# Performance work log

Measured on AMD Instinct MI355X. Metric: run time of the kernel, lower is better.

The kernel has to match this reference:

```python
import jax, jax.numpy as jnp
import numpy as np

N_NODES = 100000
N_EDGES = 1600000
IN_DIM = 256
HEADS = 4
OUT_DIM = 32
ALPHA = 0.2  # leaky relu slope


def setup_inputs() -> dict:
    key = jax.random.key(0)
    k1, k2, k3, k4, k5, k6 = jax.random.split(key, 6)
    feature = jax.random.normal(k1, (N_NODES, IN_DIM), dtype=jnp.float32)
    src = jax.random.randint(k2, (N_EDGES,), 0, N_NODES, dtype=jnp.int32)
    dst = jax.random.randint(k3, (N_EDGES,), 0, N_NODES, dtype=jnp.int32)
    W_fc = jax.random.normal(k4, (IN_DIM, HEADS * OUT_DIM), dtype=jnp.float32) * 0.05
    attn_l = jax.random.normal(k5, (1, HEADS, OUT_DIM), dtype=jnp.float32) * 0.1
    attn_r = jax.random.normal(k6, (1, HEADS, OUT_DIM), dtype=jnp.float32) * 0.1
    return {"feature": feature, "src": src, "dst": dst, "W_fc": W_fc,
            "attn_l": attn_l, "attn_r": attn_r}


def reference(feature, src, dst, W_fc, attn_l, attn_r):
    # node projection: [N, H, D]
    ft = (feature @ W_fc).reshape(feature.shape[0], HEADS, OUT_DIM)
    # per-node attention scores: [N, H]
    a1 = jnp.sum(ft * attn_l, axis=-1)
    a2 = jnp.sum(ft * attn_r, axis=-1)
    # edge attention logits: gather src/dst + leaky relu -> [E, H]
    e = a1[src] + a2[dst]
    e = jnp.where(e > 0, e, ALPHA * e)
    # segment softmax over destination groups
    n = feature.shape[0]
    e_max = jax.ops.segment_max(e, dst, num_segments=n)  # [N, H]
    e_exp = jnp.exp(e - e_max[dst])
    e_sum = jax.ops.segment_sum(e_exp, dst, num_segments=n)  # [N, H]
    alpha = e_exp / e_sum[dst]  # [E, H]
    # weighted scatter-sum aggregation: [N, H, D]
    msgs = ft[src] * alpha[:, :, None]
    out = jax.ops.segment_sum(msgs, dst, num_segments=n)
    return out
```

## Files before the change

kernel.cpp:

```cpp
#include <hip/hip_runtime.h>
#include <hip/hip_fp16.h>

#define N_NODES 100000
#define N_EDGES 1600000
#define IN_DIM 256
#define HEADS 4
#define OUT_DIM 32
#define NHD 128
#define LEAKY 0.2f

#define SCAN_BLOCK 1024
#define N_SCAN_BLOCKS ((N_NODES + SCAN_BLOCK - 1) / SCAN_BLOCK)

typedef _Float16 f16x8 __attribute__((ext_vector_type(8)));
typedef _Float16 f16x4 __attribute__((ext_vector_type(4)));
typedef float    f32x4 __attribute__((ext_vector_type(4)));

__global__ void init_kernel(int* __restrict__ deg) {
    int i = blockIdx.x * blockDim.x + threadIdx.x;
    if (i < N_NODES) deg[i] = 0;
}

__global__ void wprep_kernel(const float* __restrict__ W,
                             _Float16* __restrict__ Wt_hi,
                             _Float16* __restrict__ Wt_lo) {
    int i = blockIdx.x * blockDim.x + threadIdx.x;
    if (i < NHD * IN_DIM) {
        int c = i >> 8;
        int k = i & 255;
        float w = W[(size_t)k * NHD + c];
        _Float16 hi = (_Float16)w;
        _Float16 lo = (_Float16)(w - (float)hi);
        Wt_hi[i] = hi;
        Wt_lo[i] = lo;
    }
}

__launch_bounds__(256, 4)
__global__ void gemm_kernel(const float* __restrict__ feature,
                            const _Float16* __restrict__ Wt_hi,
                            const _Float16* __restrict__ Wt_lo,
                            const float* __restrict__ attn_l,
                            const float* __restrict__ attn_r,
                            __half* __restrict__ ft,
                            float* __restrict__ a1,
                            float* __restrict__ a2) {
    __shared__ _Float16 sA [128][40];
    __shared__ _Float16 sWh[128][40];
    __shared__ _Float16 sWl[128][40];

    const int t    = threadIdx.x;
    const int w    = t >> 6;
    const int lane = t & 63;
    const int l15  = lane & 15;
    const int kg   = lane >> 4;
    const int nb   = blockIdx.x * 128;

    f32x4 acc[8][2];
#pragma unroll
    for (int nt = 0; nt < 8; ++nt) {
        acc[nt][0] = (f32x4){0.f, 0.f, 0.f, 0.f};
        acc[nt][1] = (f32x4){0.f, 0.f, 0.f, 0.f};
    }

    for (int kt = 0; kt < 8; ++kt) {
        __syncthreads();
#pragma unroll
        for (int p = 0; p < 4; ++p) {
            int idx  = t + p * 256;
            int node = idx >> 3;
            int c4   = idx & 7;
            float4 v = make_float4(0.f, 0.f, 0.f, 0.f);
            if (nb + node < N_NODES)
                v = *(const float4*)&feature[(size_t)(nb + node) * IN_DIM + kt * 32 + c4 * 4];
            f16x4 h;
            h[0] = (_Float16)v.x; h[1] = (_Float16)v.y;
            h[2] = (_Float16)v.z; h[3] = (_Float16)v.w;
            *(f16x4*)&sA[node][c4 * 4] = h;
        }
#pragma unroll
        for (int p = 0; p < 2; ++p) {
            int c   = t + p * 256;
            int col = c >> 2;
            int kc  = c & 3;
            *(f16x8*)&sWh[col][kc * 8] =
                *(const f16x8*)&Wt_hi[(size_t)col * IN_DIM + kt * 32 + kc * 8];
            *(f16x8*)&sWl[col][kc * 8] =
                *(const f16x8*)&Wt_lo[(size_t)col * IN_DIM + kt * 32 + kc * 8];
        }
        __syncthreads();

        f16x8 wh0 = *(const f16x8*)&sWh[w * 32 + l15][kg * 8];
        f16x8 wh1 = *(const f16x8*)&sWh[w * 32 + 16 + l15][kg * 8];
        f16x8 wl0 = *(const f16x8*)&sWl[w * 32 + l15][kg * 8];
        f16x8 wl1 = *(const f16x8*)&sWl[w * 32 + 16 + l15][kg * 8];

#pragma unroll
        for (int nt = 0; nt < 8; ++nt) {
            f16x8 af = *(const f16x8*)&sA[nt * 16 + l15][kg * 8];
            acc[nt][0] = __builtin_amdgcn_mfma_f32_16x16x32_f16(wh0, af, acc[nt][0], 0, 0, 0);
            acc[nt][0] = __builtin_amdgcn_mfma_f32_16x16x32_f16(wl0, af, acc[nt][0], 0, 0, 0);
            acc[nt][1] = __builtin_amdgcn_mfma_f32_16x16x32_f16(wh1, af, acc[nt][1], 0, 0, 0);
            acc[nt][1] = __builtin_amdgcn_mfma_f32_16x16x32_f16(wl1, af, acc[nt][1], 0, 0, 0);
        }
    }

    float al8[8], ar8[8];
#pragma unroll
    for (int ct = 0; ct < 2; ++ct)
#pragma unroll
        for (int r = 0; r < 4; ++r) {
            int cb = ct * 16 + kg * 4 + r;
            al8[ct * 4 + r] = attn_l[w * 32 + cb];
            ar8[ct * 4 + r] = attn_r[w * 32 + cb];
        }

#pragma unroll
    for (int nt = 0; nt < 8; ++nt) {
        int node = nb + nt * 16 + l15;
        bool valid = node < N_NODES;
        if (valid) {
            f16x4 s0, s1;
#pragma unroll
            for (int r = 0; r < 4; ++r) {
                s0[r] = (_Float16)acc[nt][0][r];
                s1[r] = (_Float16)acc[nt][1][r];
            }
            *(f16x4*)&ft[(size_t)node * NHD + w * 32 + kg * 4]      = s0;
            *(f16x4*)&ft[(size_t)node * NHD + w * 32 + 16 + kg * 4] = s1;
        }
        float pl = 0.f, pr = 0.f;
#pragma unroll
        for (int ct = 0; ct < 2; ++ct)
#pragma unroll
            for (int r = 0; r < 4; ++r) {
                pl = fmaf(acc[nt][ct][r], al8[ct * 4 + r], pl);
                pr = fmaf(acc[nt][ct][r], ar8[ct * 4 + r], pr);
            }
        pl += __shfl_xor(pl, 16); pl += __shfl_xor(pl, 32);
        pr += __shfl_xor(pr, 16); pr += __shfl_xor(pr, 32);
        if (kg == 0 && valid) {
            a1[node * HEADS + w] = pl;
            a2[node * HEADS + w] = pr;
        }
    }
}

__global__ void hist_kernel(const int* __restrict__ dst, int* __restrict__ deg,
                            int* __restrict__ edge_pos) {
    int i = blockIdx.x * blockDim.x + threadIdx.x;
    if (i < N_EDGES) edge_pos[i] = atomicAdd(&deg[dst[i]], 1);
}

__global__ void scan1_kernel(const int* __restrict__ deg,
                             int* __restrict__ partial,
                             int* __restrict__ blocksum) {
    __shared__ int wsum[16];
    const int tid  = threadIdx.x;
    const int lane = tid & 63;
    const int wid  = tid >> 6;
    const int i    = blockIdx.x * SCAN_BLOCK + tid;
    int v = (i < N_NODES) ? deg[i] : 0;
    int x = v;
#pragma unroll
    for (int o = 1; o < 64; o <<= 1) {
        int y = __shfl_up(x, o);
        if (lane >= o) x += y;
    }
    if (lane == 63) wsum[wid] = x;
    __syncthreads();
    if (wid == 0 && lane < 16) {
        int w = wsum[lane];
#pragma unroll
        for (int o = 1; o < 16; o <<= 1) {
            int y = __shfl_up(w, o);
            if (lane >= o) w += y;
        }
        wsum[lane] = w;
    }
    __syncthreads();
    int woff = (wid > 0) ? wsum[wid - 1] : 0;
    if (i < N_NODES) partial[i] = woff + x - v;
    if (tid == SCAN_BLOCK - 1) blocksum[blockIdx.x] = wsum[15];
}

__global__ void scan2_kernel(const int* __restrict__ blocksum,
                             int* __restrict__ blockoff,
                             int* __restrict__ offsets) {
    __shared__ int wtot[2];
    const int tid  = threadIdx.x;
    const int lane = tid & 63;
    const int wid  = tid >> 6;
    int v = (tid < N_SCAN_BLOCKS) ? blocksum[tid] : 0;
    int x = v;
#pragma unroll
    for (int o = 1; o < 64; o <<= 1) {
        int y = __shfl_up(x, o);
        if (lane >= o) x += y;
    }
    if (lane == 63) wtot[wid] = x;
    __syncthreads();
    int add = (wid == 1) ? wtot[0] : 0;
    if (tid < N_SCAN_BLOCKS) blockoff[tid] = add + x - v;
    if (tid == N_SCAN_BLOCKS - 1) offsets[N_NODES] = add + x;
}

__global__ void scan3_kernel(const int* __restrict__ partial,
                             const int* __restrict__ blockoff,
                             int* __restrict__ offsets) {
    int i = blockIdx.x * SCAN_BLOCK + threadIdx.x;
    if (i < N_NODES) offsets[i] = partial[i] + blockoff[blockIdx.x];
}

__global__ void fill_kernel(const int* __restrict__ src, const int* __restrict__ dst,
                            const int* __restrict__ offsets,
                            const int* __restrict__ edge_pos,
                            int* __restrict__ src_sorted) {
    int i = blockIdx.x * blockDim.x + threadIdx.x;
    if (i < N_EDGES) {
        int idx = offsets[dst[i]] + edge_pos[i];
        src_sorted[idx] = src[i];
    }
}

__launch_bounds__(256)
__global__ void agg_kernel(const __half* __restrict__ ft,
                           const float* __restrict__ a1,
                           const float* __restrict__ a2,
                           const int* __restrict__ offsets,
                           const int* __restrict__ src_sorted,
                           float* __restrict__ out) {
    const int wave = threadIdx.x >> 6;
    const int lane = threadIdx.x & 63;
    const int node = blockIdx.x * 4 + wave;
    if (node >= N_NODES) return;
    const int h = lane >> 4;

    const float a2v = a2[node * HEADS + h];
    const int e0 = offsets[node];
    const int e1 = offsets[node + 1];

    float accx = 0.f, accy = 0.f, wsum = 0.f;
    int e = e0;

    for (; e + 3 < e1; e += 4) {
        int s0 = src_sorted[e];
        int s1 = src_sorted[e + 1];
        int s2 = src_sorted[e + 2];
        int s3 = src_sorted[e + 3];
        float b0 = a1[s0 * HEADS + h];
        float b1 = a1[s1 * HEADS + h];
        float b2 = a1[s2 * HEADS + h];
        float b3 = a1[s3 * HEADS + h];
        __half2 h0 = *(const __half2*)&ft[(size_t)s0 * NHD + lane * 2];
        __half2 h1 = *(const __half2*)&ft[(size_t)s1 * NHD + lane * 2];
        __half2 h2 = *(const __half2*)&ft[(size_t)s2 * NHD + lane * 2];
        __half2 h3 = *(const __half2*)&ft[(size_t)s3 * NHD + lane * 2];
        float2 v0 = __half22float2(h0);
        float2 v1 = __half22float2(h1);
        float2 v2 = __half22float2(h2);
        float2 v3 = __half22float2(h3);
        float ev0 = b0 + a2v; ev0 = ev0 > 0.f ? ev0 : LEAKY * ev0;
        float ev1 = b1 + a2v; ev1 = ev1 > 0.f ? ev1 : LEAKY * ev1;
        float ev2 = b2 + a2v; ev2 = ev2 > 0.f ? ev2 : LEAKY * ev2;
        float ev3 = b3 + a2v; ev3 = ev3 > 0.f ? ev3 : LEAKY * ev3;
        float w0 = __expf(ev0), w1 = __expf(ev1), w2 = __expf(ev2), w3 = __expf(ev3);
        accx = fmaf(w0, v0.x, accx); accy = fmaf(w0, v0.y, accy);
        accx = fmaf(w1, v1.x, accx); accy = fmaf(w1, v1.y, accy);
        accx = fmaf(w2, v2.x, accx); accy = fmaf(w2, v2.y, accy);
        accx = fmaf(w3, v3.x, accx); accy = fmaf(w3, v3.y, accy);
        wsum += w0 + w1 + w2 + w3;
    }
    for (; e < e1; ++e) {
        int s    = src_sorted[e];
        float ev = a1[s * HEADS + h] + a2v;
        ev       = ev > 0.f ? ev : LEAKY * ev;
        float w  = __expf(ev);
        float2 v = __half22float2(*(const __half2*)&ft[(size_t)s * NHD + lane * 2]);
        accx = fmaf(w, v.x, accx);
        accy = fmaf(w, v.y, accy);
        wsum += w;
    }
    float inv = (e1 > e0) ? 1.f / wsum : 0.f;
    float2 o = make_float2(accx * inv, accy * inv);
    *(float2*)&out[(size_t)node * NHD + lane * 2] = o;
}

extern "C" void kernel_launch(void* const* d_in, const int* in_sizes, int n_in,
                              void* d_out, int out_size, void* d_ws, size_t ws_size,
                              hipStream_t stream) {
    const float* feature = (const float*)d_in[0];
    const int*   src     = (const int*)d_in[1];
    const int*   dst     = (const int*)d_in[2];
    const float* W       = (const float*)d_in[3];
    const float* attn_l  = (const float*)d_in[4];
    const float* attn_r  = (const float*)d_in[5];
    float*       out     = (float*)d_out;

    char* ws = (char*)d_ws;
    size_t off = 0;
    auto alloc = [&](size_t bytes) -> void* {
        void* p = ws + off;
        off = (off + bytes + 255) & ~(size_t)255;
        return p;
    };
    __half*    ft        = (__half*)alloc((size_t)N_NODES * NHD * 2);
    float*     a1        = (float*)alloc((size_t)N_NODES * HEADS * 4);
    float*     a2        = (float*)alloc((size_t)N_NODES * HEADS * 4);
    int*       deg       = (int*)alloc((size_t)N_NODES * 4);
    int*       offsets   = (int*)alloc((size_t)(N_NODES + 1) * 4);
    int*       src_sorted= (int*)alloc((size_t)N_EDGES * 4);
    int*       edge_pos  = (int*)alloc((size_t)N_EDGES * 4);
    int*       partial   = (int*)alloc((size_t)N_NODES * 4);
    int*       blocksum  = (int*)alloc((size_t)N_SCAN_BLOCKS * 4);
    int*       blockoff  = (int*)alloc((size_t)N_SCAN_BLOCKS * 4);
    _Float16*  Wt_hi     = (_Float16*)alloc((size_t)NHD * IN_DIM * 2);
    _Float16*  Wt_lo     = (_Float16*)alloc((size_t)NHD * IN_DIM * 2);

    init_kernel<<<(N_NODES + 255) / 256, 256, 0, stream>>>(deg);
    wprep_kernel<<<(NHD * IN_DIM + 255) / 256, 256, 0, stream>>>(W, Wt_hi, Wt_lo);
    gemm_kernel<<<(N_NODES + 127) / 128, 256, 0, stream>>>(feature, Wt_hi, Wt_lo,
                                                           attn_l, attn_r, ft, a1, a2);
    hist_kernel<<<(N_EDGES + 255) / 256, 256, 0, stream>>>(dst, deg, edge_pos);
    scan1_kernel<<<N_SCAN_BLOCKS, SCAN_BLOCK, 0, stream>>>(deg, partial, blocksum);
    scan2_kernel<<<1, 128, 0, stream>>>(blocksum, blockoff, offsets);
    scan3_kernel<<<N_SCAN_BLOCKS, SCAN_BLOCK, 0, stream>>>(partial, blockoff, offsets);
    fill_kernel<<<(N_EDGES + 255) / 256, 256, 0, stream>>>(src, dst, offsets, edge_pos, src_sorted);
    agg_kernel<<<(N_NODES + 3) / 4, 256, 0, stream>>>(ft, a1, a2, offsets, src_sorted, out);
}
```

Before: 391.6 us.

## Pad CSR segments to multiples of four with sentinel node, vectorize index loads

Each destination's edge segment in the CSR is rounded up to a multiple of four, and the padding slots point to a sentinel node whose a1 is -1e30 and whose ft row is zero, so padded edges contribute nothing. This removes the scalar tail loop and lets the aggregation loop load four source indices with one int4 read. Attention logits are prescaled by 1/ln2 so exp2f can replace __expf, and leaky ReLU becomes fmaxf. In exchange the init kernel now writes the whole padded src_sorted buffer (about 2M ints) and the aggregation does extra gathers for padded slots.

```diff
diff --git a/kernel.cpp b/kernel.cpp
--- a/kernel.cpp
+++ b/kernel.cpp
@@ -8,6 +8,9 @@
 #define OUT_DIM 32
 #define NHD 128
 #define LEAKY 0.2f
+#define INV_LN2 1.4426950408889634f
+
+#define SS_CAP (N_EDGES + 4 * N_NODES)
 
 #define SCAN_BLOCK 1024
 #define N_SCAN_BLOCKS ((N_NODES + SCAN_BLOCK - 1) / SCAN_BLOCK)
@@ -16,9 +19,13 @@
 typedef _Float16 f16x4 __attribute__((ext_vector_type(4)));
 typedef float    f32x4 __attribute__((ext_vector_type(4)));
 
-__global__ void init_kernel(int* __restrict__ deg) {
+__global__ void init_kernel(int* __restrict__ deg, int* __restrict__ src_sorted,
+                            float* __restrict__ a1, __half* __restrict__ ft) {
     int i = blockIdx.x * blockDim.x + threadIdx.x;
     if (i < N_NODES) deg[i] = 0;
+    if (i < SS_CAP) src_sorted[i] = N_NODES;
+    if (i < HEADS) a1[N_NODES * HEADS + i] = -1e30f;
+    if (i < 64) ((unsigned*)(ft + (size_t)N_NODES * NHD))[i] = 0u;
 }
 
 __global__ void wprep_kernel(const float* __restrict__ W,
@@ -73,10 +80,10 @@
             float4 v = make_float4(0.f, 0.f, 0.f, 0.f);
             if (nb + node < N_NODES)
                 v = *(const float4*)&feature[(size_t)(nb + node) * IN_DIM + kt * 32 + c4 * 4];
-            f16x4 h;
-            h[0] = (_Float16)v.x; h[1] = (_Float16)v.y;
-            h[2] = (_Float16)v.z; h[3] = (_Float16)v.w;
-            *(f16x4*)&sA[node][c4 * 4] = h;
+            f16x4 hh;
+            hh[0] = (_Float16)v.x; hh[1] = (_Float16)v.y;
+            hh[2] = (_Float16)v.z; hh[3] = (_Float16)v.w;
+            *(f16x4*)&sA[node][c4 * 4] = hh;
         }
 #pragma unroll
         for (int p = 0; p < 2; ++p) {
@@ -140,8 +147,8 @@
         pl += __shfl_xor(pl, 16); pl += __shfl_xor(pl, 32);
         pr += __shfl_xor(pr, 16); pr += __shfl_xor(pr, 32);
         if (kg == 0 && valid) {
-            a1[node * HEADS + w] = pl;
-            a2[node * HEADS + w] = pr;
+            a1[node * HEADS + w] = pl * INV_LN2;
+            a2[node * HEADS + w] = pr * INV_LN2;
         }
     }
 }
@@ -160,7 +167,7 @@
     const int lane = tid & 63;
     const int wid  = tid >> 6;
     const int i    = blockIdx.x * SCAN_BLOCK + tid;
-    int v = (i < N_NODES) ? deg[i] : 0;
+    int v = (i < N_NODES) ? ((deg[i] + 3) & ~3) : 0;
     int x = v;
 #pragma unroll
     for (int o = 1; o < 64; o <<= 1) {
@@ -235,55 +242,42 @@
     const int node = blockIdx.x * 4 + wave;
     if (node >= N_NODES) return;
     const int h = lane >> 4;
+    const int lane2 = lane * 2;
 
     const float a2v = a2[node * HEADS + h];
     const int e0 = offsets[node];
     const int e1 = offsets[node + 1];
 
     float accx = 0.f, accy = 0.f, wsum = 0.f;
-    int e = e0;
-
-    for (; e + 3 < e1; e += 4) {
-        int s0 = src_sorted[e];
-        int s1 = src_sorted[e + 1];
-        int s2 = src_sorted[e + 2];
-        int s3 = src_sorted[e + 3];
-        float b0 = a1[s0 * HEADS + h];
-        float b1 = a1[s1 * HEADS + h];
-        float b2 = a1[s2 * HEADS + h];
-        float b3 = a1[s3 * HEADS + h];
-        __half2 h0 = *(const __half2*)&ft[(size_t)s0 * NHD + lane * 2];
-        __half2 h1 = *(const __half2*)&ft[(size_t)s1 * NHD + lane * 2];
-        __half2 h2 = *(const __half2*)&ft[(size_t)s2 * NHD + lane * 2];
-        __half2 h3 = *(const __half2*)&ft[(size_t)s3 * NHD + lane * 2];
+
+    for (int e = e0; e < e1; e += 4) {
+        int4 s4 = *(const int4*)&src_sorted[e];
+        float b0 = a1[s4.x * HEADS + h];
+        float b1 = a1[s4.y * HEADS + h];
+        float b2 = a1[s4.z * HEADS + h];
+        float b3 = a1[s4.w * HEADS + h];
+        __half2 h0 = *(const __half2*)&ft[s4.x * NHD + lane2];
+        __half2 h1 = *(const __half2*)&ft[s4.y * NHD + lane2];
+        __half2 h2 = *(const __half2*)&ft[s4.z * NHD + lane2];
+        __half2 h3 = *(const __half2*)&ft[s4.w * NHD + lane2];
+        float t0 = b0 + a2v, t1 = b1 + a2v, t2 = b2 + a2v, t3 = b3 + a2v;
+        float w0 = exp2f(fmaxf(t0, LEAKY * t0));
+        float w1 = exp2f(fmaxf(t1, LEAKY * t1));
+        float w2 = exp2f(fmaxf(t2, LEAKY * t2));
+        float w3 = exp2f(fmaxf(t3, LEAKY * t3));
         float2 v0 = __half22float2(h0);
         float2 v1 = __half22float2(h1);
         float2 v2 = __half22float2(h2);
         float2 v3 = __half22float2(h3);
-        float ev0 = b0 + a2v; ev0 = ev0 > 0.f ? ev0 : LEAKY * ev0;
-        float ev1 = b1 + a2v; ev1 = ev1 > 0.f ? ev1 : LEAKY * ev1;
-        float ev2 = b2 + a2v; ev2 = ev2 > 0.f ? ev2 : LEAKY * ev2;
-        float ev3 = b3 + a2v; ev3 = ev3 > 0.f ? ev3 : LEAKY * ev3;
-        float w0 = __expf(ev0), w1 = __expf(ev1), w2 = __expf(ev2), w3 = __expf(ev3);
         accx = fmaf(w0, v0.x, accx); accy = fmaf(w0, v0.y, accy);
         accx = fmaf(w1, v1.x, accx); accy = fmaf(w1, v1.y, accy);
         accx = fmaf(w2, v2.x, accx); accy = fmaf(w2, v2.y, accy);
         accx = fmaf(w3, v3.x, accx); accy = fmaf(w3, v3.y, accy);
-        wsum += w0 + w1 + w2 + w3;
-    }
-    for (; e < e1; ++e) {
-        int s    = src_sorted[e];
-        float ev = a1[s * HEADS + h] + a2v;
-        ev       = ev > 0.f ? ev : LEAKY * ev;
-        float w  = __expf(ev);
-        float2 v = __half22float2(*(const __half2*)&ft[(size_t)s * NHD + lane * 2]);
-        accx = fmaf(w, v.x, accx);
-        accy = fmaf(w, v.y, accy);
-        wsum += w;
+        wsum += (w0 + w1) + (w2 + w3);
     }
     float inv = (e1 > e0) ? 1.f / wsum : 0.f;
     float2 o = make_float2(accx * inv, accy * inv);
-    *(float2*)&out[(size_t)node * NHD + lane * 2] = o;
+    *(float2*)&out[(size_t)node * NHD + lane2] = o;
 }
 
 extern "C" void kernel_launch(void* const* d_in, const int* in_sizes, int n_in,
@@ -304,12 +298,12 @@
         off = (off + bytes + 255) & ~(size_t)255;
         return p;
     };
-    __half*    ft        = (__half*)alloc((size_t)N_NODES * NHD * 2);
-    float*     a1        = (float*)alloc((size_t)N_NODES * HEADS * 4);
+    __half*    ft        = (__half*)alloc((size_t)(N_NODES + 1) * NHD * 2);
+    float*     a1        = (float*)alloc((size_t)(N_NODES + 1) * HEADS * 4);
     float*     a2        = (float*)alloc((size_t)N_NODES * HEADS * 4);
     int*       deg       = (int*)alloc((size_t)N_NODES * 4);
     int*       offsets   = (int*)alloc((size_t)(N_NODES + 1) * 4);
-    int*       src_sorted= (int*)alloc((size_t)N_EDGES * 4);
+    int*       src_sorted= (int*)alloc((size_t)SS_CAP * 4);
     int*       edge_pos  = (int*)alloc((size_t)N_EDGES * 4);
     int*       partial   = (int*)alloc((size_t)N_NODES * 4);
     int*       blocksum  = (int*)alloc((size_t)N_SCAN_BLOCKS * 4);
@@ -317,7 +311,7 @@
     _Float16*  Wt_hi     = (_Float16*)alloc((size_t)NHD * IN_DIM * 2);
     _Float16*  Wt_lo     = (_Float16*)alloc((size_t)NHD * IN_DIM * 2);
 
-    init_kernel<<<(N_NODES + 255) / 256, 256, 0, stream>>>(deg);
+    init_kernel<<<(SS_CAP + 255) / 256, 256, 0, stream>>>(deg, src_sorted, a1, ft);
     wprep_kernel<<<(NHD * IN_DIM + 255) / 256, 256, 0, stream>>>(W, Wt_hi, Wt_lo);
     gemm_kernel<<<(N_NODES + 127) / 128, 256, 0, stream>>>(feature, Wt_hi, Wt_lo,
                                                            attn_l, attn_r, ft, a1, a2);
```

After: 396.9 us. About the same (+1.4%).
